# Performance work log

Hardware: AMD Instinct MI355X
Metric: run time of the kernel (lower is better)

## Reference

```python
import jax, jax.numpy as jnp
import numpy as np

B, D_K, D_V = 1024, 64, 64
N_FEAT, RANK, K = 32768, 1, 32

def _normalize(a):
    return a / jnp.linalg.norm(a, axis=-1, keepdims=True)

def setup_inputs() -> dict:
    key = jax.random.key(0)
    k0, k1, k2, k3, k4 = jax.random.split(key, 5)
    x = jax.random.normal(k0, (B, D_K, D_V), dtype=jnp.float32)
    V_enc = _normalize(jax.random.normal(k1, (N_FEAT, RANK, D_K), dtype=jnp.float32))
    W_enc = _normalize(jax.random.normal(k2, (N_FEAT, RANK, D_V), dtype=jnp.float32))
    V_dec = _normalize(jax.random.normal(k3, (N_FEAT, RANK, D_K), dtype=jnp.float32))
    W_dec = _normalize(jax.random.normal(k4, (N_FEAT, RANK, D_V), dtype=jnp.float32))
    b_enc = jnp.zeros((N_FEAT,), dtype=jnp.float32)
    bias = jnp.zeros((D_K, D_V), dtype=jnp.float32)
    return {"x": x, "V_enc": V_enc, "W_enc": W_enc, "b_enc": b_enc,
            "V_dec": V_dec, "W_dec": W_dec, "bias": bias}

def reference(x, V_enc, W_enc, b_enc, V_dec, W_dec, bias):
    b, d_k, d_v = x.shape
    n_feat = V_enc.shape[0]
    x_flat = x.reshape(b, d_k * d_v)
    # encode: einsum('irk,bkv,irv->bi') == x_flat @ (sum_r v_ir (x) w_ir)^T
    M_enc = jnp.einsum('irk,irv->ikv', V_enc, W_enc).reshape(n_feat, d_k * d_v)
    pre = x_flat @ M_enc.T + b_enc                       # [B, n_feat]
    # topk activation with relu on the kept values, zeros elsewhere
    vals, idx = jax.lax.top_k(pre, K)                    # [B, K]
    vals = jnp.maximum(vals, 0.0)
    coeffs = jnp.zeros_like(pre).at[jnp.arange(b)[:, None], idx].set(vals)
    # decode: einsum('bi,irk,irv->bkv')
    M_dec = jnp.einsum('irk,irv->ikv', V_dec, W_dec).reshape(n_feat, d_k * d_v)
    recon_flat = coeffs @ M_dec + bias.reshape(-1)
    recon = recon_flat.reshape(b, d_k, d_v)
    mse = jnp.mean((recon_flat - x_flat) ** 2)
    # fresh steps_since_active buffer (zeros) + dead_threshold=100 -> no dead
    # features, so aux_loss == 0 exactly; total loss == mse.
    return recon, coeffs, mse
```

## Files before the change

kernel.cpp:

```cpp
#include <hip/hip_runtime.h>
#include <hip/hip_bf16.h>
#include <hip/hip_fp8.h>
#include <stdint.h>

#define NFEAT 32768
#define BATCH 1024
#define DK 64
#define DV 64
#define DD 4096
#define KSEL 32
#define CAND_CAP 512
#define CAND_TARGET 128

using bf16 = __bf16;
using f32x4 = __attribute__((ext_vector_type(4))) float;
using f32x16 = __attribute__((ext_vector_type(16))) float;
using i32x4 = __attribute__((ext_vector_type(4))) int;
using i32x8 = __attribute__((ext_vector_type(8))) int;

__device__ __forceinline__ void gload_lds16(const void* g, void* l) {
  __builtin_amdgcn_global_load_lds((const __attribute__((address_space(1))) void*)g,
                                   (__attribute__((address_space(3))) void*)l,
                                   16, 0, 0);
}

__device__ inline unsigned mono16(unsigned u) {
  return (u & 0x8000u) ? ((~u) & 0xFFFFu) : (u | 0x8000u);
}


__global__ void k_convert_x(const float* __restrict__ x, unsigned char* __restrict__ xb) {
  int t = threadIdx.x;
  int rb = blockIdx.x >> 3;
  int kg0 = (blockIdx.x & 7) * 16;
  int row = (t & 127) >> 2;
  int cin = ((t >> 7) << 4) + ((t & 3) << 2);
  const float* xrow = x + ((size_t)rb * 32 + row) * DD;
  for (int kg = kg0; kg < kg0 + 16; ++kg) {
    float4 v = *reinterpret_cast<const float4*>(xrow + kg * 32 + cin);
    union { unsigned char b[4]; unsigned u; } o;
    o.b[0] = __hip_fp8_e4m3(v.x).__x;
    o.b[1] = __hip_fp8_e4m3(v.y).__x;
    o.b[2] = __hip_fp8_e4m3(v.z).__x;
    o.b[3] = __hip_fp8_e4m3(v.w).__x;
    *reinterpret_cast<unsigned*>(xb + (((size_t)rb * 128 + kg) << 10) + t * 4) = o.u;
  }
}

__global__ void k_build_menc(const float* __restrict__ Venc, const float* __restrict__ Wenc,
                             unsigned char* __restrict__ Menc) {
  int t = threadIdx.x;
  int rb = blockIdx.x;
  int row = (t & 127) >> 2;
  int cin = ((t >> 7) << 4) + ((t & 3) << 2);
  size_t rowg = (size_t)rb * 32 + row;
  const float* vrow = Venc + rowg * DK;
  float4 w0 = *reinterpret_cast<const float4*>(Wenc + rowg * DV + cin);
  float4 w1 = *reinterpret_cast<const float4*>(Wenc + rowg * DV + 32 + cin);
  unsigned char* base = Menc + ((size_t)rb << 17);
#pragma unroll 4
  for (int kg = 0; kg < 128; ++kg) {
    float vk = 16.0f * vrow[kg >> 1];
    float4 w = (kg & 1) ? w1 : w0;
    union { unsigned char b[4]; unsigned u; } o;
    o.b[0] = __hip_fp8_e4m3(vk * w.x).__x;
    o.b[1] = __hip_fp8_e4m3(vk * w.y).__x;
    o.b[2] = __hip_fp8_e4m3(vk * w.z).__x;
    o.b[3] = __hip_fp8_e4m3(vk * w.w).__x;
    *reinterpret_cast<unsigned*>(base + (kg << 10) + t * 4) = o.u;
  }
}

#define BM 256
#define BN 256
#define BKB 128
#define NT (DD / BKB)
#define ABUF 32768
#define BUFSZ 65536
#define GEMM_LDS (2 * BUFSZ)

__device__ __forceinline__ void stage_chunk(const unsigned char* __restrict__ G, size_t r32base,
                                            int kg0, int c, int lane, char* dstbase) {
  const unsigned char* src = G + (((r32base + (c >> 2)) * 128 + kg0 + (c & 3)) << 10) + lane * 16;
  gload_lds16(src, dstbase + c * 1024);
}

__device__ __forceinline__ i32x8 frag_ld8(const char* base, int chunk, int lane) {
  const char* p = base + chunk * 1024 + (lane & 31) * 16;
  i32x4 lo = *reinterpret_cast<const i32x4*>(p);
  i32x4 hi = *reinterpret_cast<const i32x4*>(p + 512);
  i32x8 r;
  r[0] = lo[0]; r[1] = lo[1]; r[2] = lo[2]; r[3] = lo[3];
  r[4] = hi[0]; r[5] = hi[1]; r[6] = hi[2]; r[7] = hi[3];
  return r;
}

__device__ __forceinline__ int chA(int half, int idx) {
  int g = idx >> 2, kg = idx & 3;
  int mb32 = (g & 1) + ((g >> 1) << 2) + half * 2;
  return mb32 * 4 + kg;
}
__device__ __forceinline__ int chB(int half, int idx) {
  int nb32 = ((idx >> 2) << 1) + half;
  return nb32 * 4 + (idx & 3);
}

#define LD_A(H)                                                                     \
  _Pragma("unroll") for (int mb = 0; mb < 2; ++mb)                                  \
  _Pragma("unroll") for (int kh = 0; kh < 2; ++kh)                                  \
    afr[mb][kh] = frag_ld8(cur, (wr * 4 + (H) * 2 + mb) * 4 + kh * 2 + (lane >> 5), lane);

#define LD_B(H)                                                                     \
  _Pragma("unroll") for (int kh = 0; kh < 2; ++kh)                                  \
    bfr[(H)][kh] = frag_ld8(cur + ABUF, (wc * 2 + (H)) * 4 + kh * 2 + (lane >> 5), lane);

#define ST_A(HALF, KT)                                                              \
  stage_chunk(A, ar32, (KT) * 4, chA(HALF, wave * 2), lane, nxt);                   \
  stage_chunk(A, ar32, (KT) * 4, chA(HALF, wave * 2 + 1), lane, nxt);

#define ST_B(HALF, KT)                                                              \
  stage_chunk(Bt, br32, (KT) * 4, chB(HALF, wave * 2), lane, nxt + ABUF);           \
  stage_chunk(Bt, br32, (KT) * 4, chB(HALF, wave * 2 + 1), lane, nxt + ABUF);

#define MFMA_Q(MH, NB)                                                              \
  asm volatile("s_waitcnt lgkmcnt(0)" ::: "memory");                                \
  __builtin_amdgcn_sched_barrier(0);                                                \
  __builtin_amdgcn_s_setprio(1);                                                    \
  _Pragma("unroll") for (int mb = 0; mb < 2; ++mb)                                  \
  _Pragma("unroll") for (int kh = 0; kh < 2; ++kh)                                  \
    acc[(MH) * 2 + mb][NB] = __builtin_amdgcn_mfma_scale_f32_32x32x64_f8f6f4(       \
        afr[mb][kh], bfr[NB][kh], acc[(MH) * 2 + mb][NB], 0, 0, 0, 0x7F, 0, 0x7F);  \
  __builtin_amdgcn_s_setprio(0);

#define VMC(N) asm volatile("s_waitcnt vmcnt(" #N ")" ::: "memory");
#define LGKM0 asm volatile("s_waitcnt lgkmcnt(0)" ::: "memory");
#define BARR                                                                        \
  asm volatile("s_barrier" ::: "memory");                                           \
  __builtin_amdgcn_sched_barrier(0);

__global__ __launch_bounds__(512, 2)
void k_gemm(const unsigned char* __restrict__ A, const unsigned char* __restrict__ Bt,
            const float* __restrict__ benc, bf16* __restrict__ C) {
  extern __shared__ char lds[];
  int tid = threadIdx.x;
  int wave = tid >> 6;
  int lane = tid & 63;
  int wr = wave >> 2;
  int wc = wave & 3;

  int d = blockIdx.x;
  int lw = (d & 7) * 64 + (d >> 3);
  int q = lw >> 2;
  int p = lw & 3;
  size_t brow = (size_t)p * BM;
  size_t bcol = (size_t)q * BN;
  size_t ar32 = brow >> 5;
  size_t br32 = bcol >> 5;

  f32x16 acc[4][2] = {};
  i32x8 afr[2][2];
  i32x8 bfr[2][2];

  {
    char* nxt = lds;
    ST_B(0, 0) ST_A(0, 0) ST_B(1, 0) ST_A(1, 0)
  }
  VMC(2)
  BARR

#pragma unroll 1
  for (int u = 0; u < NT - 1; ++u) {
    char* cur = lds + (u & 1) * BUFSZ;
    char* nxt = lds + ((u + 1) & 1) * BUFSZ;
    int k1 = u + 1;
    LD_A(0) LD_B(0) LD_B(1)
    ST_B(0, k1) ST_A(0, k1) ST_B(1, k1)
    VMC(6)
    BARR
    MFMA_Q(0, 0)
    MFMA_Q(0, 1)
    LD_A(1)
    ST_A(1, k1)
    VMC(2)
    LGKM0
    BARR
    MFMA_Q(1, 1)
    MFMA_Q(1, 0)
  }

  {
    char* cur = lds + ((NT - 1) & 1) * BUFSZ;
    LD_A(0) LD_B(0) LD_B(1)
    VMC(0)
    BARR
    MFMA_Q(0, 0)
    MFMA_Q(0, 1)
    LD_A(1)
    MFMA_Q(1, 1)
    MFMA_Q(1, 0)
  }

#pragma unroll
  for (int nb = 0; nb < 2; ++nb) {
    size_t col = bcol + wc * 64 + nb * 32 + (lane & 31);
    float be = benc[col];
#pragma unroll
    for (int MB = 0; MB < 4; ++MB) {
      size_t row0 = brow + wr * 128 + MB * 32 + ((lane >> 5) << 2);
#pragma unroll
      for (int reg = 0; reg < 16; ++reg) {
        size_t row = row0 + (reg & 3) + ((reg >> 2) << 3);
        C[row * NFEAT + col] = (bf16)(acc[MB][nb][reg] * 0.0625f + be);
      }
    }
  }
}

#define HIDX(b) (((b) & 31) * 257 + ((b) >> 5))
#define HSIZE (32 * 257)

__global__ __launch_bounds__(256, 4)
void k_select(const unsigned short* __restrict__ pre,
              const float* __restrict__ x,
              const float* __restrict__ Venc,
              const float* __restrict__ Wenc,
              const float* __restrict__ benc,
              const float* __restrict__ Vdec,
              const float* __restrict__ Wdec,
              const float* __restrict__ bias,
              float* __restrict__ recon,
              float* __restrict__ coeffs,
              float* __restrict__ msepart) {
  __shared__ __align__(16) int hist[HSIZE];
  __shared__ int wtot[4];
  __shared__ int sBstar;
  __shared__ int scount;
  __shared__ float rval[CAND_CAP];
  __shared__ int ridx[CAND_CAP];
  __shared__ float selv[KSEL];
  __shared__ int seli[KSEL];
  __shared__ float red[256];
  float (*Vd)[DK] = (float(*)[DK])hist;
  float (*Wd)[DV] = (float(*)[DV])(hist + 2048);

  int b = blockIdx.x;
  int t = threadIdx.x;
  int wave = t >> 6;
  int lane = t & 63;

  const unsigned short* row = pre + (size_t)b * NFEAT;
  const float* xr = x + (size_t)b * DD;
  float* crow = coeffs + (size_t)b * NFEAT;

  float xreg[DK];
#pragma unroll
  for (int kk = 0; kk < DK; ++kk)
    xreg[kk] = xr[kk * DV + lane];

  for (int i = t; i < HSIZE; i += 256) hist[i] = 0;
  if (t == 0) scount = 0;
  __syncthreads();

  float4 z4 = {0.f, 0.f, 0.f, 0.f};
  for (int i = (t << 3); i < NFEAT; i += 2048) {
    uint4 v = *reinterpret_cast<const uint4*>(row + i);
#pragma unroll
    for (int j = 0; j < 4; ++j) {
      unsigned w = (&v.x)[j];
      atomicAdd(&hist[HIDX(mono16(w & 0xFFFFu) >> 3)], 1);
      atomicAdd(&hist[HIDX(mono16(w >> 16) >> 3)], 1);
    }
    *reinterpret_cast<float4*>(crow + i) = z4;
    *reinterpret_cast<float4*>(crow + i + 4) = z4;
  }
  __syncthreads();

  int s = 0;
#pragma unroll
  for (int i = 0; i < 32; ++i) s += hist[i * 257 + t];
  int rsum = s;
#pragma unroll
  for (int off = 1; off < 64; off <<= 1) {
    int v = __shfl_down(rsum, off);
    rsum += (lane + off < 64) ? v : 0;
  }
  if (lane == 0) wtot[wave] = rsum;
  __syncthreads();
  int hiw = 0;
#pragma unroll
  for (int w2 = 0; w2 < 4; ++w2)
    hiw += (w2 > wave) ? wtot[w2] : 0;
  int suff = (rsum - s) + hiw;
  if (suff < CAND_TARGET && suff + s >= CAND_TARGET) {
    int acc = suff;
    int bstar = t * 32;
    for (int i = 31; i >= 0; --i) {
      acc += hist[i * 257 + t];
      if (acc >= CAND_TARGET) { bstar = t * 32 + i; break; }
    }
    sBstar = bstar;
  }
  __syncthreads();
  int Bstar = sBstar;

  for (int i = (t << 3); i < NFEAT; i += 2048) {
    uint4 v = *reinterpret_cast<const uint4*>(row + i);
#pragma unroll
    for (int j = 0; j < 4; ++j) {
      unsigned w = (&v.x)[j];
      int b0 = (int)(mono16(w & 0xFFFFu) >> 3);
      int b1 = (int)(mono16(w >> 16) >> 3);
      if (b0 >= Bstar) { int p2 = atomicAdd(&scount, 1); if (p2 < CAND_CAP) ridx[p2] = i + j * 2; }
      if (b1 >= Bstar) { int p2 = atomicAdd(&scount, 1); if (p2 < CAND_CAP) ridx[p2] = i + j * 2 + 1; }
    }
  }
  __syncthreads();
  int c = scount;
  if (c > CAND_CAP) c = CAND_CAP;

  for (int j = wave; j < c; j += 4) {
    int fi = __builtin_amdgcn_readfirstlane(ridx[j]);
    const float* vr = Venc + (size_t)fi * DK;
    float w = Wenc[(size_t)fi * DV + lane];
    float a0 = 0.f, a1 = 0.f, a2 = 0.f, a3 = 0.f;
#pragma unroll
    for (int kk = 0; kk < DK; kk += 4) {
      a0 = fmaf(xreg[kk + 0], vr[kk + 0], a0);
      a1 = fmaf(xreg[kk + 1], vr[kk + 1], a1);
      a2 = fmaf(xreg[kk + 2], vr[kk + 2], a2);
      a3 = fmaf(xreg[kk + 3], vr[kk + 3], a3);
    }
    float p2 = ((a0 + a1) + (a2 + a3)) * w;
#pragma unroll
    for (int off = 1; off < 64; off <<= 1) p2 += __shfl_xor(p2, off);
    if (lane == 0) rval[j] = p2 + benc[fi];
  }
  __syncthreads();

  for (int t2 = t; t2 < c; t2 += 256) {
    float v = rval[t2];
    int fi = ridx[t2];
    int rank = 0;
    for (int j = 0; j < c; ++j) {
      float vj = rval[j];
      if (vj > v || (vj == v && ridx[j] < fi)) ++rank;
    }
    if (rank < KSEL) { selv[rank] = v; seli[rank] = fi; }
  }
  __syncthreads();

  if (t < KSEL) {
    float v = fmaxf(selv[t], 0.f);
    selv[t] = v;
    crow[seli[t]] = v;
  }
  __syncthreads();

  for (int i = t; i < KSEL * DK; i += 256) {
    int s2 = i >> 6, e = i & 63;
    Vd[s2][e] = Vdec[(size_t)seli[s2] * DK + e];
    Wd[s2][e] = Wdec[(size_t)seli[s2] * DV + e];
  }
  __syncthreads();

  int k = t >> 2;
  int vb = (t & 3) << 4;
  float4 r4[4];
#pragma unroll
  for (int g = 0; g < 4; ++g)
    r4[g] = *reinterpret_cast<const float4*>(bias + k * DV + vb + g * 4);
#pragma unroll
  for (int s2 = 0; s2 < KSEL; ++s2) {
    float a = selv[s2] * Vd[s2][k];
    const float4* wrow = reinterpret_cast<const float4*>(&Wd[s2][vb]);
#pragma unroll
    for (int g = 0; g < 4; ++g) {
      float4 wv = wrow[g];
      r4[g].x = fmaf(a, wv.x, r4[g].x);
      r4[g].y = fmaf(a, wv.y, r4[g].y);
      r4[g].z = fmaf(a, wv.z, r4[g].z);
      r4[g].w = fmaf(a, wv.w, r4[g].w);
    }
  }
  float m = 0.f;
  float* ro = recon + (size_t)b * DD + k * DV + vb;
#pragma unroll
  for (int g = 0; g < 4; ++g) {
    float4 xv = *reinterpret_cast<const float4*>(xr + k * DV + vb + g * 4);
    float dx = r4[g].x - xv.x, dy = r4[g].y - xv.y;
    float dz = r4[g].z - xv.z, dw = r4[g].w - xv.w;
    m = fmaf(dx, dx, m); m = fmaf(dy, dy, m);
    m = fmaf(dz, dz, m); m = fmaf(dw, dw, m);
    *reinterpret_cast<float4*>(ro + g * 4) = r4[g];
  }
  red[t] = m;
  __syncthreads();
  for (int s2 = 128; s2 > 0; s2 >>= 1) {
    if (t < s2) red[t] += red[t + s2];
    __syncthreads();
  }
  if (t == 0) msepart[b] = red[0];
}

__global__ void k_mse(const float* __restrict__ msepart, float* __restrict__ out) {
  __shared__ float red[256];
  int t = threadIdx.x;
  float s = 0.f;
  for (int i = t; i < BATCH; i += 256) s += msepart[i];
  red[t] = s;
  __syncthreads();
  for (int k = 128; k > 0; k >>= 1) {
    if (t < k) red[t] += red[t + k];
    __syncthreads();
  }
  if (t == 0) out[0] = red[0] / (float)((size_t)BATCH * DD);
}

extern "C" void kernel_launch(void* const* d_in, const int* in_sizes, int n_in,
                              void* d_out, int out_size, void* d_ws, size_t ws_size,
                              hipStream_t stream) {
  const float* x    = (const float*)d_in[0];
  const float* Venc = (const float*)d_in[1];
  const float* Wenc = (const float*)d_in[2];
  const float* benc = (const float*)d_in[3];
  const float* Vdec = (const float*)d_in[4];
  const float* Wdec = (const float*)d_in[5];
  const float* bias = (const float*)d_in[6];

  float* out = (float*)d_out;
  float* recon  = out;
  float* coeffs = out + (size_t)BATCH * DD;
  float* mse    = coeffs + (size_t)BATCH * NFEAT;

  char* wsp = (char*)d_ws;
  unsigned char* xb8 = (unsigned char*)wsp;   wsp += (size_t)BATCH * DD;
  unsigned char* Menc8 = (unsigned char*)wsp; wsp += (size_t)NFEAT * DD;
  float* msepart = (float*)wsp;               wsp += (size_t)BATCH * sizeof(float);
  bf16* pre = (bf16*)wsp;                     wsp += (size_t)BATCH * NFEAT * sizeof(bf16);

  hipFuncSetAttribute((const void*)k_gemm, hipFuncAttributeMaxDynamicSharedMemorySize,
                      GEMM_LDS);

  k_convert_x<<<256, 256, 0, stream>>>(x, xb8);
  k_build_menc<<<NFEAT / 32, 256, 0, stream>>>(Venc, Wenc, Menc8);
  k_gemm<<<(BATCH / BM) * (NFEAT / BN), 512, GEMM_LDS, stream>>>(xb8, Menc8, benc, pre);
  k_select<<<BATCH, 256, 0, stream>>>((const unsigned short*)pre, x, Venc, Wenc, benc,
                                      Vdec, Wdec, bias, recon, coeffs, msepart);
  k_mse<<<1, 256, 0, stream>>>(msepart, mse);
}
```

Baseline: 307.1 us.

## Split select kernel into histogram top-k and refine kernels, zero coeffs separately

The monolithic select kernel is split into a light histogram/candidate kernel and a register-heavy refine kernel that rescores candidates in fp32, selects the top-k and decodes. Candidate indices are passed through a global workspace buffer. The zeroing of the 128MB coeffs output moves to a dedicated kernel. The goal is higher occupancy for the histogram pass, which no longer has to hold 64 x values in registers. It costs an extra launch and some global traffic for candidates. A barrier is also added in the GEMM epilogue before the last MFMA group, apparently to fix an LDS race.

```diff
diff --git a/kernel.cpp b/kernel.cpp
--- a/kernel.cpp
+++ b/kernel.cpp
@@ -26,6 +26,14 @@
 
 __device__ inline unsigned mono16(unsigned u) {
   return (u & 0x8000u) ? ((~u) & 0xFFFFu) : (u | 0x8000u);
+}
+
+__global__ void k_zero(float* __restrict__ coeffs) {
+  size_t base = ((size_t)blockIdx.x * 256 + threadIdx.x) * 64;
+  float4 z4 = {0.f, 0.f, 0.f, 0.f};
+#pragma unroll
+  for (int i = 0; i < 16; ++i)
+    *reinterpret_cast<float4*>(coeffs + base + i * 4) = z4;
 }
 
 
@@ -196,6 +204,8 @@
     MFMA_Q(0, 0)
     MFMA_Q(0, 1)
     LD_A(1)
+    LGKM0
+    BARR
     MFMA_Q(1, 1)
     MFMA_Q(1, 0)
   }
@@ -219,49 +229,21 @@
 #define HIDX(b) (((b) & 31) * 257 + ((b) >> 5))
 #define HSIZE (32 * 257)
 
-__global__ __launch_bounds__(256, 4)
-void k_select(const unsigned short* __restrict__ pre,
-              const float* __restrict__ x,
-              const float* __restrict__ Venc,
-              const float* __restrict__ Wenc,
-              const float* __restrict__ benc,
-              const float* __restrict__ Vdec,
-              const float* __restrict__ Wdec,
-              const float* __restrict__ bias,
-              float* __restrict__ recon,
-              float* __restrict__ coeffs,
-              float* __restrict__ msepart) {
+__global__ void k_topk(const unsigned short* __restrict__ pre, int* __restrict__ cand_idx,
+                       int* __restrict__ cand_cnt) {
   __shared__ __align__(16) int hist[HSIZE];
   __shared__ int wtot[4];
   __shared__ int sBstar;
   __shared__ int scount;
-  __shared__ float rval[CAND_CAP];
-  __shared__ int ridx[CAND_CAP];
-  __shared__ float selv[KSEL];
-  __shared__ int seli[KSEL];
-  __shared__ float red[256];
-  float (*Vd)[DK] = (float(*)[DK])hist;
-  float (*Wd)[DV] = (float(*)[DV])(hist + 2048);
-
   int b = blockIdx.x;
   int t = threadIdx.x;
   int wave = t >> 6;
   int lane = t & 63;
-
   const unsigned short* row = pre + (size_t)b * NFEAT;
-  const float* xr = x + (size_t)b * DD;
-  float* crow = coeffs + (size_t)b * NFEAT;
-
-  float xreg[DK];
-#pragma unroll
-  for (int kk = 0; kk < DK; ++kk)
-    xreg[kk] = xr[kk * DV + lane];
-
   for (int i = t; i < HSIZE; i += 256) hist[i] = 0;
   if (t == 0) scount = 0;
   __syncthreads();
 
-  float4 z4 = {0.f, 0.f, 0.f, 0.f};
   for (int i = (t << 3); i < NFEAT; i += 2048) {
     uint4 v = *reinterpret_cast<const uint4*>(row + i);
 #pragma unroll
@@ -270,8 +252,6 @@
       atomicAdd(&hist[HIDX(mono16(w & 0xFFFFu) >> 3)], 1);
       atomicAdd(&hist[HIDX(mono16(w >> 16) >> 3)], 1);
     }
-    *reinterpret_cast<float4*>(crow + i) = z4;
-    *reinterpret_cast<float4*>(crow + i + 4) = z4;
   }
   __syncthreads();
 
@@ -302,6 +282,7 @@
   }
   __syncthreads();
   int Bstar = sBstar;
+  int* cidx = cand_idx + b * CAND_CAP;
 
   for (int i = (t << 3); i < NFEAT; i += 2048) {
     uint4 v = *reinterpret_cast<const uint4*>(row + i);
@@ -310,14 +291,53 @@
       unsigned w = (&v.x)[j];
       int b0 = (int)(mono16(w & 0xFFFFu) >> 3);
       int b1 = (int)(mono16(w >> 16) >> 3);
-      if (b0 >= Bstar) { int p2 = atomicAdd(&scount, 1); if (p2 < CAND_CAP) ridx[p2] = i + j * 2; }
-      if (b1 >= Bstar) { int p2 = atomicAdd(&scount, 1); if (p2 < CAND_CAP) ridx[p2] = i + j * 2 + 1; }
-    }
-  }
-  __syncthreads();
-  int c = scount;
+      if (b0 >= Bstar) { int p2 = atomicAdd(&scount, 1); if (p2 < CAND_CAP) cidx[p2] = i + j * 2; }
+      if (b1 >= Bstar) { int p2 = atomicAdd(&scount, 1); if (p2 < CAND_CAP) cidx[p2] = i + j * 2 + 1; }
+    }
+  }
+  __syncthreads();
+  if (t == 0) cand_cnt[b] = (scount < CAND_CAP) ? scount : CAND_CAP;
+}
+
+__global__ __launch_bounds__(256, 2)
+void k_refine(const float* __restrict__ x,
+              const float* __restrict__ Venc,
+              const float* __restrict__ Wenc,
+              const float* __restrict__ benc,
+              const float* __restrict__ Vdec,
+              const float* __restrict__ Wdec,
+              const float* __restrict__ bias,
+              const int* __restrict__ cand_idx,
+              const int* __restrict__ cand_cnt,
+              float* __restrict__ recon,
+              float* __restrict__ coeffs,
+              float* __restrict__ msepart) {
+  __shared__ float rval[CAND_CAP];
+  __shared__ int ridx[CAND_CAP];
+  __shared__ float selv[KSEL];
+  __shared__ int seli[KSEL];
+  __shared__ float Vd[KSEL][DK];
+  __shared__ float Wd[KSEL][DV];
+  __shared__ float red[256];
+
+  int b = blockIdx.x;
+  int t = threadIdx.x;
+  int wave = t >> 6;
+  int lane = t & 63;
+
+  const float* xr = x + (size_t)b * DD;
+
+  int c = cand_cnt[b];
   if (c > CAND_CAP) c = CAND_CAP;
-
+  for (int i = t; i < c; i += 256) ridx[i] = cand_idx[b * CAND_CAP + i];
+  __syncthreads();
+
+  float xreg[DK];
+#pragma unroll
+  for (int kk = 0; kk < DK; ++kk)
+    xreg[kk] = xr[kk * DV + lane];
+
+#pragma unroll 2
   for (int j = wave; j < c; j += 4) {
     int fi = __builtin_amdgcn_readfirstlane(ridx[j]);
     const float* vr = Venc + (size_t)fi * DK;
@@ -352,7 +372,7 @@
   if (t < KSEL) {
     float v = fmaxf(selv[t], 0.f);
     selv[t] = v;
-    crow[seli[t]] = v;
+    coeffs[(size_t)b * NFEAT + seli[t]] = v;
   }
   __syncthreads();
 
@@ -435,16 +455,20 @@
   char* wsp = (char*)d_ws;
   unsigned char* xb8 = (unsigned char*)wsp;   wsp += (size_t)BATCH * DD;
   unsigned char* Menc8 = (unsigned char*)wsp; wsp += (size_t)NFEAT * DD;
+  int* cand_idx = (int*)wsp;                  wsp += (size_t)BATCH * CAND_CAP * sizeof(int);
+  int* cand_cnt = (int*)wsp;                  wsp += (size_t)BATCH * sizeof(int);
   float* msepart = (float*)wsp;               wsp += (size_t)BATCH * sizeof(float);
   bf16* pre = (bf16*)wsp;                     wsp += (size_t)BATCH * NFEAT * sizeof(bf16);
 
   hipFuncSetAttribute((const void*)k_gemm, hipFuncAttributeMaxDynamicSharedMemorySize,
                       GEMM_LDS);
 
+  k_zero<<<(BATCH * NFEAT) / (256 * 64), 256, 0, stream>>>(coeffs);
   k_convert_x<<<256, 256, 0, stream>>>(x, xb8);
   k_build_menc<<<NFEAT / 32, 256, 0, stream>>>(Venc, Wenc, Menc8);
   k_gemm<<<(BATCH / BM) * (NFEAT / BN), 512, GEMM_LDS, stream>>>(xb8, Menc8, benc, pre);
-  k_select<<<BATCH, 256, 0, stream>>>((const unsigned short*)pre, x, Venc, Wenc, benc,
-                                      Vdec, Wdec, bias, recon, coeffs, msepart);
+  k_topk<<<BATCH, 256, 0, stream>>>((const unsigned short*)pre, cand_idx, cand_cnt);
+  k_refine<<<BATCH, 256, 0, stream>>>(x, Venc, Wenc, benc, Vdec, Wdec, bias,
+                                      cand_idx, cand_cnt, recon, coeffs, msepart);
   k_mse<<<1, 256, 0, stream>>>(msepart, mse);
 }
```

Result: slower. 320.0 us (+4.2%).
